# Performance work log

Measured on AMD Instinct MI355X. Metric: run time of the kernel, lower is better.

Reference implementation:

```python
import jax, jax.numpy as jnp
import numpy as np

B, C, H, W = 16, 256, 64, 64
DA = 64  # attention_size


def setup_inputs() -> dict:
    key = jax.random.key(0)
    ks = jax.random.split(key, 7)
    s_in = 1.0 / np.sqrt(C)
    return {
        "x": jax.random.normal(ks[0], (B, C, H, W), jnp.float32),
        "Wq": jax.random.normal(ks[1], (DA, C), jnp.float32) * s_in,
        "bq": jax.random.normal(ks[2], (DA,), jnp.float32) * 0.01,
        "Wk": jax.random.normal(ks[3], (DA, C), jnp.float32) * s_in,
        "bk": jax.random.normal(ks[4], (DA,), jnp.float32) * 0.01,
        "Wv": jax.random.normal(ks[5], (C, C), jnp.float32) * s_in,
        "bv": jax.random.normal(ks[6], (C,), jnp.float32) * 0.01,
    }


def reference(x, Wq, bq, Wk, bk, Wv, bv):
    b, c, h, w = x.shape
    n = h * w
    xf = x.reshape(b, c, n)                      # [B,C,N]
    q = jnp.einsum('ac,bcn->ban', Wq, xf) + bq[None, :, None]   # [B,DA,N]
    k = jnp.einsum('ac,bcn->ban', Wk, xf) + bk[None, :, None]   # [B,DA,N]
    v = jnp.einsum('dc,bcn->bdn', Wv, xf) + bv[None, :, None]   # [B,C,N]
    # scores[b,i,j] = q[:,i] . k[:,j], scaled by 1/sqrt(H*W) (as in source)
    scores = jnp.einsum('bai,baj->bij', q, k) / jnp.sqrt(jnp.float32(n))
    attn = jax.nn.softmax(scores, axis=-1)       # [B,N,N]
    out = jnp.einsum('bcj,bij->bci', v, attn)    # [B,C,N]
    return out.reshape(b, c, h, w) + x
```

## Files before the change

### kernel.cpp

```cpp
#include <hip/hip_runtime.h>
#include <hip/hip_bf16.h>
#include <stdint.h>


#define B_  16
#define C_  256
#define N_  4096
#define DA_ 64
#define MSHIFT 2.0f

typedef __attribute__((ext_vector_type(8))) short short8;
typedef __attribute__((ext_vector_type(4))) float f32x4;

__device__ int g_isf32;

__device__ __forceinline__ short f2bf(float f) {
    union { float f; uint32_t u; } v; v.f = f;
    uint32_t r = v.u + 0x7fffu + ((v.u >> 16) & 1u);
    return (short)(r >> 16);
}
__device__ __forceinline__ float bf2f(uint16_t s) {
    union { uint32_t u; float f; } v; v.u = ((uint32_t)s) << 16;
    return v.f;
}
__device__ __forceinline__ uint32_t pkbf(float a, float b) {
    union { __hip_bfloat162 h; uint32_t u; } c;
    c.h = __float22bfloat162_rn(make_float2(a, b));
    return c.u;
}

__global__ void detect_kernel(const void* __restrict__ x) {
    const uint16_t* p = (const uint16_t*)x;
    int i = threadIdx.x;
    uint16_t u = p[2 * i];
    int e = (u >> 7) & 0xFF;
    unsigned long long m = __ballot(e >= 112 && e <= 132);
    if (i == 0) g_isf32 = (__popcll(m) < 32) ? 1 : 0;
}

template<bool F32>
__device__ __forceinline__ void proj_body(
    const void* __restrict__ xv,
    const void* __restrict__ Wqv, const void* __restrict__ bqv,
    const void* __restrict__ Wkv, const void* __restrict__ bkv,
    const void* __restrict__ Wvv, const void* __restrict__ bvv,
    uint16_t* __restrict__ Q, uint16_t* __restrict__ K, uint16_t* __restrict__ Vt,
    float* bias_lds, uint16_t* buf)
{
    const int tid = threadIdx.x;
    const int b  = blockIdx.x >> 6;
    const int n0 = (blockIdx.x & 63) * 64;
    const int w = tid >> 6, lane = tid & 63, q = lane >> 4, ln = lane & 15;

    for (int idx = tid; idx < 384; idx += 256) {
        float bias;
        if (F32) {
            bias = (idx < 64)  ? ((const float*)bqv)[idx]
                 : (idx < 128) ? ((const float*)bkv)[idx - 64]
                               : ((const float*)bvv)[idx - 128];
        } else {
            bias = (idx < 64)  ? bf2f(((const uint16_t*)bqv)[idx])
                 : (idx < 128) ? bf2f(((const uint16_t*)bkv)[idx - 64])
                               : bf2f(((const uint16_t*)bvv)[idx - 128]);
        }
        bias_lds[idx] = bias;
    }

    {
        int cbase = tid >> 2, s0 = tid & 3;
        #pragma unroll
        for (int cc = 0; cc < 4; cc++) {
            int c = cc * 64 + cbase;
            if (F32) {
                const float* xr = (const float*)xv + ((size_t)b * C_ + c) * N_ + n0;
                #pragma unroll
                for (int k = 0; k < 4; k++) {
                    int nl = (s0 + 4 * k) * 4;
                    float4 v = *(const float4*)(xr + nl);
                    buf[(nl + 0) * 264 + c] = (uint16_t)f2bf(v.x);
                    buf[(nl + 1) * 264 + c] = (uint16_t)f2bf(v.y);
                    buf[(nl + 2) * 264 + c] = (uint16_t)f2bf(v.z);
                    buf[(nl + 3) * 264 + c] = (uint16_t)f2bf(v.w);
                }
            } else {
                const uint16_t* xr = (const uint16_t*)xv + ((size_t)b * C_ + c) * N_ + n0;
                #pragma unroll
                for (int k = 0; k < 2; k++) {
                    int nl = s0 * 16 + k * 8;
                    short8 v = *(const short8*)(xr + nl);
                    #pragma unroll
                    for (int e = 0; e < 8; e++)
                        buf[(nl + e) * 264 + c] = (uint16_t)v[e];
                }
            }
        }
    }
    __syncthreads();

    f32x4 acc[6][4];
    #pragma unroll
    for (int mt = 0; mt < 6; mt++)
        #pragma unroll
        for (int nt = 0; nt < 4; nt++) acc[mt][nt] = (f32x4)0.0f;

    for (int kc = 0; kc < 8; kc++) {
        short8 af[6];
        #pragma unroll
        for (int mt = 0; mt < 6; mt++) {
            int row = (w * 6 + mt) * 16 + ln;
            if (F32) {
                const float* src = (row < 64) ? (const float*)Wqv + (size_t)row * 256
                                 : (row < 128) ? (const float*)Wkv + (size_t)(row - 64) * 256
                                               : (const float*)Wvv + (size_t)(row - 128) * 256;
                float4 a0 = *(const float4*)(src + kc * 32 + q * 8);
                float4 a1 = *(const float4*)(src + kc * 32 + q * 8 + 4);
                union { short8 s; uint32_t u[4]; } c;
                c.u[0] = pkbf(a0.x, a0.y); c.u[1] = pkbf(a0.z, a0.w);
                c.u[2] = pkbf(a1.x, a1.y); c.u[3] = pkbf(a1.z, a1.w);
                af[mt] = c.s;
            } else {
                const uint16_t* src = (row < 64) ? (const uint16_t*)Wqv + (size_t)row * 256
                                    : (row < 128) ? (const uint16_t*)Wkv + (size_t)(row - 64) * 256
                                                  : (const uint16_t*)Wvv + (size_t)(row - 128) * 256;
                af[mt] = *(const short8*)(src + kc * 32 + q * 8);
            }
        }
        short8 bfr[4];
        #pragma unroll
        for (int nt = 0; nt < 4; nt++)
            bfr[nt] = *(const short8*)&buf[(nt * 16 + ln) * 264 + kc * 32 + q * 8];
        #pragma unroll
        for (int mt = 0; mt < 6; mt++)
            #pragma unroll
            for (int nt = 0; nt < 4; nt++)
                acc[mt][nt] = __builtin_amdgcn_mfma_f32_16x16x32_bf16(
                    af[mt], bfr[nt], acc[mt][nt], 0, 0, 0);
    }
    __syncthreads();

    #pragma unroll
    for (int mt = 0; mt < 6; mt++) {
        int rowb = (w * 6 + mt) * 16 + q * 4;
        #pragma unroll
        for (int r = 0; r < 4; r++) {
            float bias = bias_lds[rowb + r];
            #pragma unroll
            for (int nt = 0; nt < 4; nt++)
                buf[(rowb + r) * 72 + nt * 16 + ln] =
                    (uint16_t)f2bf(acc[mt][nt][r] + bias);
        }
    }
    __syncthreads();

    {
        int a = tid & 63, nb = tid >> 6;
        uint16_t* Qb = Q + ((size_t)b * N_ + n0) * 64;
        uint16_t* Kb = K + ((size_t)b * N_ + n0) * 64;
        #pragma unroll 4
        for (int j = 0; j < 16; j++) {
            int n = nb + 4 * j;
            Qb[(size_t)n * 64 + a] = buf[a * 72 + n];
            Kb[(size_t)n * 64 + a] = buf[(64 + a) * 72 + n];
        }
    }
    {
        int ch = tid & 7;
        #pragma unroll
        for (int p = 0; p < 8; p++) {
            int c = p * 32 + (tid >> 3);
            short8 v = *(const short8*)&buf[(128 + c) * 72 + ch * 8];
            *(short8*)(Vt + ((size_t)b * C_ + c) * N_ + n0 + ch * 8) = v;
        }
    }
}

__global__ __launch_bounds__(256, 2) void proj_kernel(
    const void* xv, const void* Wqv, const void* bqv, const void* Wkv,
    const void* bkv, const void* Wvv, const void* bvv,
    uint16_t* Q, uint16_t* K, uint16_t* Vt)
{
    __shared__ float    bias_lds[384];
    __shared__ uint16_t buf[384 * 72];
    if (g_isf32) proj_body<true >(xv, Wqv, bqv, Wkv, bkv, Wvv, bvv, Q, K, Vt, bias_lds, buf);
    else         proj_body<false>(xv, Wqv, bqv, Wkv, bkv, Wvv, bvv, Q, K, Vt, bias_lds, buf);
}

template<bool F32>
__device__ __forceinline__ void flash_body(
    const uint16_t* __restrict__ Q, const uint16_t* __restrict__ K,
    const uint16_t* __restrict__ Vt, const void* __restrict__ xv,
    void* __restrict__ outv,
    uint16_t* Klds2, uint16_t* Plds2, float* l_lds)
{
    const int tid = threadIdx.x;
    const int d  = blockIdx.x;
    const int xc = d & 7, kk = d >> 3;
    const int b  = xc + ((kk >= 32) ? 8 : 0);
    const int i0 = (kk & 31) * 128;
    const int w = tid >> 6, lane = tid & 63, q = lane >> 4, ln = lane & 15;
    const int rw = w >> 2, cw = w & 3;

    const float c1 = 1.4426950408889634f / 64.0f;

    short8 qf[2];
    {
        const uint16_t* qrow = Q + ((size_t)b * N_ + (i0 + w * 16 + ln)) * 64;
        qf[0] = *(const short8*)(qrow + q * 8);
        qf[1] = *(const short8*)(qrow + 32 + q * 8);
    }

    const uint16_t* Kb = K + (size_t)b * N_ * 64;
    const uint16_t* vr0 = Vt + ((size_t)b * C_ + (cw * 64 +  0 + ln)) * N_ + q * 8;
    const uint16_t* vr1 = Vt + ((size_t)b * C_ + (cw * 64 + 16 + ln)) * N_ + q * 8;
    const uint16_t* vr2 = Vt + ((size_t)b * C_ + (cw * 64 + 32 + ln)) * N_ + q * 8;
    const uint16_t* vr3 = Vt + ((size_t)b * C_ + (cw * 64 + 48 + ln)) * N_ + q * 8;

    const int krow = tid >> 3, kch = (tid & 7) * 8;

    float l_run = 0.0f;
    f32x4 O[4][4];
    #pragma unroll
    for (int rg = 0; rg < 4; rg++)
        #pragma unroll
        for (int ct = 0; ct < 4; ct++) O[rg][ct] = (f32x4)0.0f;

    {
        short8 k0 = *(const short8*)(Kb + (size_t)krow * 64 + kch);
        *(short8*)&Klds2[krow * 72 + kch] = k0;
    }
    __syncthreads();

    for (int it = 0; it < 64; it++) {
        const int j0 = it * 64;
        const int cur = it & 1;
        const uint16_t* Kc = Klds2 + cur * (64 * 72);
        uint16_t*       Kn = Klds2 + (cur ^ 1) * (64 * 72);
        uint16_t*       Pl = Plds2 + cur * (128 * 72);

        short8 v00 = *(const short8*)(vr0 + j0);
        short8 v01 = *(const short8*)(vr1 + j0);
        short8 v02 = *(const short8*)(vr2 + j0);
        short8 v03 = *(const short8*)(vr3 + j0);
        short8 v10 = *(const short8*)(vr0 + j0 + 32);
        short8 v11 = *(const short8*)(vr1 + j0 + 32);
        short8 v12 = *(const short8*)(vr2 + j0 + 32);
        short8 v13 = *(const short8*)(vr3 + j0 + 32);

        short8 kreg;
        if (it < 63)
            kreg = *(const short8*)(Kb + (size_t)(j0 + 64 + krow) * 64 + kch);

        f32x4 s[4];
        #pragma unroll
        for (int jt = 0; jt < 4; jt++) s[jt] = (f32x4)0.0f;
        #pragma unroll
        for (int jt = 0; jt < 4; jt++) {
            short8 kf0 = *(const short8*)&Kc[(jt * 16 + ln) * 72 + q * 8];
            s[jt] = __builtin_amdgcn_mfma_f32_16x16x32_bf16(kf0, qf[0], s[jt], 0, 0, 0);
            short8 kf1 = *(const short8*)&Kc[(jt * 16 + ln) * 72 + 32 + q * 8];
            s[jt] = __builtin_amdgcn_mfma_f32_16x16x32_bf16(kf1, qf[1], s[jt], 0, 0, 0);
        }

        uint16_t* prow = &Pl[(w * 16 + ln) * 72 + q * 4];
        #pragma unroll
        for (int jt = 0; jt < 4; jt++) {
            float p0 = exp2f(s[jt][0] * c1 - MSHIFT);
            float p1 = exp2f(s[jt][1] * c1 - MSHIFT);
            float p2 = exp2f(s[jt][2] * c1 - MSHIFT);
            float p3 = exp2f(s[jt][3] * c1 - MSHIFT);
            l_run += (p0 + p1) + (p2 + p3);
            uint2 pk; pk.x = pkbf(p0, p1); pk.y = pkbf(p2, p3);
            *(uint2*)&prow[jt * 16] = pk;
        }

        asm volatile("s_waitcnt lgkmcnt(0)\n\ts_barrier" ::: "memory");

        {
            short8 af[4];
            #pragma unroll
            for (int rg = 0; rg < 4; rg++)
                af[rg] = *(const short8*)&Pl[(rw * 64 + rg * 16 + ln) * 72 + q * 8];
            #pragma unroll
            for (int rg = 0; rg < 4; rg++) {
                O[rg][0] = __builtin_amdgcn_mfma_f32_16x16x32_bf16(af[rg], v00, O[rg][0], 0, 0, 0);
                O[rg][1] = __builtin_amdgcn_mfma_f32_16x16x32_bf16(af[rg], v01, O[rg][1], 0, 0, 0);
                O[rg][2] = __builtin_amdgcn_mfma_f32_16x16x32_bf16(af[rg], v02, O[rg][2], 0, 0, 0);
                O[rg][3] = __builtin_amdgcn_mfma_f32_16x16x32_bf16(af[rg], v03, O[rg][3], 0, 0, 0);
            }
            #pragma unroll
            for (int rg = 0; rg < 4; rg++)
                af[rg] = *(const short8*)&Pl[(rw * 64 + rg * 16 + ln) * 72 + 32 + q * 8];
            #pragma unroll
            for (int rg = 0; rg < 4; rg++) {
                O[rg][0] = __builtin_amdgcn_mfma_f32_16x16x32_bf16(af[rg], v10, O[rg][0], 0, 0, 0);
                O[rg][1] = __builtin_amdgcn_mfma_f32_16x16x32_bf16(af[rg], v11, O[rg][1], 0, 0, 0);
                O[rg][2] = __builtin_amdgcn_mfma_f32_16x16x32_bf16(af[rg], v12, O[rg][2], 0, 0, 0);
                O[rg][3] = __builtin_amdgcn_mfma_f32_16x16x32_bf16(af[rg], v13, O[rg][3], 0, 0, 0);
            }
        }

        if (it < 63) {
            asm volatile("s_waitcnt vmcnt(0)" ::: "memory");
            *(short8*)&Kn[krow * 72 + kch] = kreg;
        }
        asm volatile("s_waitcnt lgkmcnt(0)\n\ts_barrier" ::: "memory");
    }

    l_run += __shfl_xor(l_run, 16);
    l_run += __shfl_xor(l_run, 32);
    if (lane < 16) l_lds[w * 16 + lane] = l_run;
    __syncthreads();

    #pragma unroll
    for (int rg = 0; rg < 4; rg++) {
        f32x4 lv = *(const f32x4*)&l_lds[rw * 64 + rg * 16 + q * 4];
        f32x4 li; li[0] = 1.0f/lv[0]; li[1] = 1.0f/lv[1]; li[2] = 1.0f/lv[2]; li[3] = 1.0f/lv[3];
        #pragma unroll
        for (int ct = 0; ct < 4; ct++) {
            int c = cw * 64 + ct * 16 + ln;
            size_t off = (size_t)c * N_ + i0 + rw * 64 + rg * 16 + q * 4;
            if (F32) {
                const float* xb = (const float*)xv + (size_t)b * C_ * N_;
                float* ob = (float*)outv + (size_t)b * C_ * N_;
                float4 xv4 = *(const float4*)(xb + off);
                float4 res;
                res.x = O[rg][ct][0] * li[0] + xv4.x;
                res.y = O[rg][ct][1] * li[1] + xv4.y;
                res.z = O[rg][ct][2] * li[2] + xv4.z;
                res.w = O[rg][ct][3] * li[3] + xv4.w;
                *(float4*)(ob + off) = res;
            } else {
                const uint16_t* xb = (const uint16_t*)xv + (size_t)b * C_ * N_;
                uint16_t* ob = (uint16_t*)outv + (size_t)b * C_ * N_;
                uint2 xp = *(const uint2*)(xb + off);
                uint2 res;
                res.x = pkbf(O[rg][ct][0] * li[0] + bf2f((uint16_t)(xp.x & 0xFFFF)),
                             O[rg][ct][1] * li[1] + bf2f((uint16_t)(xp.x >> 16)));
                res.y = pkbf(O[rg][ct][2] * li[2] + bf2f((uint16_t)(xp.y & 0xFFFF)),
                             O[rg][ct][3] * li[3] + bf2f((uint16_t)(xp.y >> 16)));
                *(uint2*)(ob + off) = res;
            }
        }
    }
}

__global__ __launch_bounds__(512, 2) void flash_kernel(
    const uint16_t* Q, const uint16_t* K, const uint16_t* Vt,
    const void* xv, void* outv)
{
    __shared__ uint16_t Klds2[2 * 64 * 72];
    __shared__ uint16_t Plds2[2 * 128 * 72];
    __shared__ __align__(16) float l_lds[128];
    if (g_isf32) flash_body<true >(Q, K, Vt, xv, outv, Klds2, Plds2, l_lds);
    else         flash_body<false>(Q, K, Vt, xv, outv, Klds2, Plds2, l_lds);
}

extern "C" void kernel_launch(void* const* d_in, const int* in_sizes, int n_in,
                              void* d_out, int out_size, void* d_ws, size_t ws_size,
                              hipStream_t stream) {
    const void* x  = d_in[0];
    const void* Wq = d_in[1];
    const void* bq = d_in[2];
    const void* Wk = d_in[3];
    const void* bk = d_in[4];
    const void* Wv = d_in[5];
    const void* bv = d_in[6];

    uint16_t* Qw = (uint16_t*)d_ws;
    uint16_t* Kw = Qw + (size_t)B_ * N_ * DA_;
    uint16_t* Vw = Kw + (size_t)B_ * N_ * DA_;

    detect_kernel<<<dim3(1), dim3(64), 0, stream>>>(x);
    proj_kernel<<<dim3(B_ * 64), dim3(256), 0, stream>>>(x, Wq, bq, Wk, bk, Wv, bv, Qw, Kw, Vw);
    flash_kernel<<<dim3(B_ * 32), dim3(512), 0, stream>>>(Qw, Kw, Vw, x, d_out);
}
```

Before: 482.4 us.

## Halve flash block query tile to 64 rows with 4 waves and 1024 blocks

Each flash block now handles 64 query rows with 256 threads (4 waves) instead of 128 rows with 512 threads, and the grid doubles to 1024 blocks. Each wave owns 64 output channels for all 64 rows, and each thread loads two short8 chunks of K per tile. This is meant to improve load balance across CUs (512 blocks is only about two per CU) and raise occupancy, with launch bounds changed to 256 threads and 3 blocks. In exchange, K and V are read twice as often per query row, since each K/V tile is reused across fewer queries.

```diff
diff --git a/kernel.cpp b/kernel.cpp
--- a/kernel.cpp
+++ b/kernel.cpp
@@ -194,11 +194,10 @@
 {
     const int tid = threadIdx.x;
     const int d  = blockIdx.x;
-    const int xc = d & 7, kk = d >> 3;
-    const int b  = xc + ((kk >= 32) ? 8 : 0);
-    const int i0 = (kk & 31) * 128;
+    const int xc = d & 7, rest = d >> 3;
+    const int b  = xc + ((rest >= 64) ? 8 : 0);
+    const int i0 = (rest & 63) * 64;
     const int w = tid >> 6, lane = tid & 63, q = lane >> 4, ln = lane & 15;
-    const int rw = w >> 2, cw = w & 3;
 
     const float c1 = 1.4426950408889634f / 64.0f;
 
@@ -210,12 +209,12 @@
     }
 
     const uint16_t* Kb = K + (size_t)b * N_ * 64;
-    const uint16_t* vr0 = Vt + ((size_t)b * C_ + (cw * 64 +  0 + ln)) * N_ + q * 8;
-    const uint16_t* vr1 = Vt + ((size_t)b * C_ + (cw * 64 + 16 + ln)) * N_ + q * 8;
-    const uint16_t* vr2 = Vt + ((size_t)b * C_ + (cw * 64 + 32 + ln)) * N_ + q * 8;
-    const uint16_t* vr3 = Vt + ((size_t)b * C_ + (cw * 64 + 48 + ln)) * N_ + q * 8;
-
-    const int krow = tid >> 3, kch = (tid & 7) * 8;
+    const uint16_t* vr0 = Vt + ((size_t)b * C_ + (w * 64 +  0 + ln)) * N_ + q * 8;
+    const uint16_t* vr1 = Vt + ((size_t)b * C_ + (w * 64 + 16 + ln)) * N_ + q * 8;
+    const uint16_t* vr2 = Vt + ((size_t)b * C_ + (w * 64 + 32 + ln)) * N_ + q * 8;
+    const uint16_t* vr3 = Vt + ((size_t)b * C_ + (w * 64 + 48 + ln)) * N_ + q * 8;
+
+    const int krow = tid >> 2, kch = (tid & 3) * 16;
 
     float l_run = 0.0f;
     f32x4 O[4][4];
@@ -226,7 +225,9 @@
 
     {
         short8 k0 = *(const short8*)(Kb + (size_t)krow * 64 + kch);
-        *(short8*)&Klds2[krow * 72 + kch] = k0;
+        short8 k1 = *(const short8*)(Kb + (size_t)krow * 64 + kch + 8);
+        *(short8*)&Klds2[krow * 72 + kch]     = k0;
+        *(short8*)&Klds2[krow * 72 + kch + 8] = k1;
     }
     __syncthreads();
 
@@ -235,7 +236,7 @@
         const int cur = it & 1;
         const uint16_t* Kc = Klds2 + cur * (64 * 72);
         uint16_t*       Kn = Klds2 + (cur ^ 1) * (64 * 72);
-        uint16_t*       Pl = Plds2 + cur * (128 * 72);
+        uint16_t*       Pl = Plds2 + cur * (64 * 72);
 
         short8 v00 = *(const short8*)(vr0 + j0);
         short8 v01 = *(const short8*)(vr1 + j0);
@@ -246,9 +247,11 @@
         short8 v12 = *(const short8*)(vr2 + j0 + 32);
         short8 v13 = *(const short8*)(vr3 + j0 + 32);
 
-        short8 kreg;
-        if (it < 63)
-            kreg = *(const short8*)(Kb + (size_t)(j0 + 64 + krow) * 64 + kch);
+        short8 kreg0, kreg1;
+        if (it < 63) {
+            kreg0 = *(const short8*)(Kb + (size_t)(j0 + 64 + krow) * 64 + kch);
+            kreg1 = *(const short8*)(Kb + (size_t)(j0 + 64 + krow) * 64 + kch + 8);
+        }
 
         f32x4 s[4];
         #pragma unroll
@@ -279,7 +282,7 @@
             short8 af[4];
             #pragma unroll
             for (int rg = 0; rg < 4; rg++)
-                af[rg] = *(const short8*)&Pl[(rw * 64 + rg * 16 + ln) * 72 + q * 8];
+                af[rg] = *(const short8*)&Pl[(rg * 16 + ln) * 72 + q * 8];
             #pragma unroll
             for (int rg = 0; rg < 4; rg++) {
                 O[rg][0] = __builtin_amdgcn_mfma_f32_16x16x32_bf16(af[rg], v00, O[rg][0], 0, 0, 0);
@@ -289,7 +292,7 @@
             }
             #pragma unroll
             for (int rg = 0; rg < 4; rg++)
-                af[rg] = *(const short8*)&Pl[(rw * 64 + rg * 16 + ln) * 72 + 32 + q * 8];
+                af[rg] = *(const short8*)&Pl[(rg * 16 + ln) * 72 + 32 + q * 8];
             #pragma unroll
             for (int rg = 0; rg < 4; rg++) {
                 O[rg][0] = __builtin_amdgcn_mfma_f32_16x16x32_bf16(af[rg], v10, O[rg][0], 0, 0, 0);
@@ -301,7 +304,8 @@
 
         if (it < 63) {
             asm volatile("s_waitcnt vmcnt(0)" ::: "memory");
-            *(short8*)&Kn[krow * 72 + kch] = kreg;
+            *(short8*)&Kn[krow * 72 + kch]     = kreg0;
+            *(short8*)&Kn[krow * 72 + kch + 8] = kreg1;
         }
         asm volatile("s_waitcnt lgkmcnt(0)\n\ts_barrier" ::: "memory");
     }
@@ -313,12 +317,12 @@
 
     #pragma unroll
     for (int rg = 0; rg < 4; rg++) {
-        f32x4 lv = *(const f32x4*)&l_lds[rw * 64 + rg * 16 + q * 4];
+        f32x4 lv = *(const f32x4*)&l_lds[rg * 16 + q * 4];
         f32x4 li; li[0] = 1.0f/lv[0]; li[1] = 1.0f/lv[1]; li[2] = 1.0f/lv[2]; li[3] = 1.0f/lv[3];
         #pragma unroll
         for (int ct = 0; ct < 4; ct++) {
-            int c = cw * 64 + ct * 16 + ln;
-            size_t off = (size_t)c * N_ + i0 + rw * 64 + rg * 16 + q * 4;
+            int c = w * 64 + ct * 16 + ln;
+            size_t off = (size_t)c * N_ + i0 + rg * 16 + q * 4;
             if (F32) {
                 const float* xb = (const float*)xv + (size_t)b * C_ * N_;
                 float* ob = (float*)outv + (size_t)b * C_ * N_;
@@ -344,13 +348,13 @@
     }
 }
 
-__global__ __launch_bounds__(512, 2) void flash_kernel(
+__global__ __launch_bounds__(256, 3) void flash_kernel(
     const uint16_t* Q, const uint16_t* K, const uint16_t* Vt,
     const void* xv, void* outv)
 {
     __shared__ uint16_t Klds2[2 * 64 * 72];
-    __shared__ uint16_t Plds2[2 * 128 * 72];
-    __shared__ __align__(16) float l_lds[128];
+    __shared__ uint16_t Plds2[2 * 64 * 72];
+    __shared__ __align__(16) float l_lds[64];
     if (g_isf32) flash_body<true >(Q, K, Vt, xv, outv, Klds2, Plds2, l_lds);
     else         flash_body<false>(Q, K, Vt, xv, outv, Klds2, Plds2, l_lds);
 }
@@ -372,5 +376,5 @@
 
     detect_kernel<<<dim3(1), dim3(64), 0, stream>>>(x);
     proj_kernel<<<dim3(B_ * 64), dim3(256), 0, stream>>>(x, Wq, bq, Wk, bk, Wv, bv, Qw, Kw, Vw);
-    flash_kernel<<<dim3(B_ * 32), dim3(512), 0, stream>>>(Qw, Kw, Vw, x, d_out);
-}
+    flash_kernel<<<dim3(B_ * 64), dim3(256), 0, stream>>>(Qw, Kw, Vw, x, d_out);
+}
```

New measurement: 442.7 us. 1.09x faster.
